# Kernel tuning notes

Measured on AMD Instinct MI355X. Metric: run time of the kernel, lower is better.

Reference implementation:

```python
import jax, jax.numpy as jnp
import numpy as np

B, S, E, H, NE, TOPK = 8, 1024, 768, 12, 8, 2
F = 4 * E
DH = E // H

def _ln(x, g, b, eps=1e-5):
    m = jnp.mean(x, axis=-1, keepdims=True)
    v = jnp.mean((x - m) ** 2, axis=-1, keepdims=True)
    return (x - m) / jnp.sqrt(v + eps) * g + b

def _expert(x, lg, lb, w1, b1, w2, b2):
    # Expert: LayerNorm -> Linear(E,4E) -> GELU(exact) -> Linear(4E,E); dropout is identity in eval
    h = _ln(x, lg, lb)
    h = jax.nn.gelu(h @ w1.T + b1, approximate=False)
    return h @ w2.T + b2

def setup_inputs():
    key = jax.random.key(0)
    ks = jax.random.split(key, 16)
    rn = lambda k, shape, s=0.02: jax.random.normal(k, shape, jnp.float32) * s
    return {
        'x': jax.random.normal(ks[0], (B, S, E), jnp.float32),
        'modality_type': jax.random.randint(ks[1], (B, S), 0, 2).astype(jnp.int32),
        'norm1_g': jnp.ones((E,), jnp.float32), 'norm1_b': jnp.zeros((E,), jnp.float32),
        'norm2_g': jnp.ones((E,), jnp.float32), 'norm2_b': jnp.zeros((E,), jnp.float32),
        'in_proj_w': rn(ks[2], (3 * E, E)), 'in_proj_b': jnp.zeros((3 * E,), jnp.float32),
        'out_proj_w': rn(ks[3], (E, E)), 'out_proj_b': jnp.zeros((E,), jnp.float32),
        'router_w': rn(ks[4], (NE, E)), 'router_b': jnp.zeros((NE,), jnp.float32),
        'spec_ln_g': jnp.ones((3, E), jnp.float32), 'spec_ln_b': jnp.zeros((3, E), jnp.float32),
        'spec_w1': rn(ks[5], (3, F, E)), 'spec_b1': jnp.zeros((3, F), jnp.float32),
        'spec_w2': rn(ks[6], (3, E, F)), 'spec_b2': jnp.zeros((3, E), jnp.float32),
        'gen_ln_g': jnp.ones((NE, E), jnp.float32), 'gen_ln_b': jnp.zeros((NE, E), jnp.float32),
        'gen_w1': rn(ks[7], (NE, F, E)), 'gen_b1': jnp.zeros((NE, F), jnp.float32),
        'gen_w2': rn(ks[8], (NE, E, F)), 'gen_b2': jnp.zeros((NE, E), jnp.float32),
    }

def _forward(x, modality_type, norm1_g, norm1_b, norm2_g, norm2_b, in_proj_w, in_proj_b,
             out_proj_w, out_proj_b, router_w, router_b,
             spec_ln_g, spec_ln_b, spec_w1, spec_b1, spec_w2, spec_b2,
             gen_ln_g, gen_ln_b, gen_w1, gen_b1, gen_w2, gen_b2):
    # --- self-attention block (pre-norm + residual), matches nn.MultiheadAttention ---
    residual = x
    xn = _ln(x, norm1_g, norm1_b)
    qkv = xn @ in_proj_w.T + in_proj_b                          # [B,S,3E]
    q, k, v = jnp.split(qkv, 3, axis=-1)
    q = q.reshape(B, S, H, DH); k = k.reshape(B, S, H, DH); v = v.reshape(B, S, H, DH)
    scores = jnp.einsum('bqhd,bkhd->bhqk', q, k) / jnp.sqrt(jnp.float32(DH))
    attn = jax.nn.softmax(scores, axis=-1)
    ctx = jnp.einsum('bhqk,bkhd->bqhd', attn, v).reshape(B, S, E)
    x = residual + (ctx @ out_proj_w.T + out_proj_b)

    # --- MoE block (pre-norm + residual) ---
    residual = x
    xn = _ln(x, norm2_g, norm2_b)
    expert_out = _expert(xn, spec_ln_g[0], spec_ln_b[0], spec_w1[0], spec_b1[0], spec_w2[0], spec_b2[0])
    # modality experts: vision on tokens with type==0, text on type==1 (not a fusion layer)
    vmask = (modality_type == 0).astype(xn.dtype)[..., None]
    tmask = (modality_type == 1).astype(xn.dtype)[..., None]
    expert_out = expert_out + vmask * _expert(xn, spec_ln_g[1], spec_ln_b[1], spec_w1[1], spec_b1[1], spec_w2[1], spec_b2[1])
    expert_out = expert_out + tmask * _expert(xn, spec_ln_g[2], spec_ln_b[2], spec_w1[2], spec_b1[2], spec_w2[2], spec_b2[2])

    # --- router: softmax -> top_k -> renormalize over top_k ---
    logits = xn @ router_w.T + router_b                         # [B,S,NE]
    probs = jax.nn.softmax(logits, axis=-1)
    topk_probs, topk_idx = jax.lax.top_k(probs, TOPK)
    topk_w = jax.nn.softmax(topk_probs, axis=-1)                # [B,S,TOPK]

    # --- dispatch/combine: per-expert combine coefficient; experts are per-token so
    # dense masked compute is mathematically identical to the torch gather/scatter loop ---
    for e in range(NE):
        coef = jnp.sum(topk_w * (topk_idx == e), axis=-1)[..., None]   # [B,S,1]
        expert_out = expert_out + coef * _expert(xn, gen_ln_g[e], gen_ln_b[e], gen_w1[e], gen_b1[e], gen_w2[e], gen_b2[e])

    return residual + expert_out

def reference(x, modality_type, norm1_g, norm1_b, norm2_g, norm2_b, in_proj_w, in_proj_b,
              out_proj_w, out_proj_b, router_w, router_b,
              spec_ln_g, spec_ln_b, spec_w1, spec_b1, spec_w2, spec_b2,
              gen_ln_g, gen_ln_b, gen_w1, gen_b1, gen_w2, gen_b2):
    return _forward(x, modality_type, norm1_g, norm1_b, norm2_g, norm2_b, in_proj_w, in_proj_b,
                    out_proj_w, out_proj_b, router_w, router_b,
                    spec_ln_g, spec_ln_b, spec_w1, spec_b1, spec_w2, spec_b2,
                    gen_ln_g, gen_ln_b, gen_w1, gen_b1, gen_w2, gen_b2)
```

## Files before the change

### kernel.cpp

```cpp
#include <hip/hip_runtime.h>
#include <cstdint>

#define NTOK 8192
#define EDIM 768
#define FDIM 3072

using bf16x8 = __attribute__((ext_vector_type(8))) __bf16;
using f32x4  = __attribute__((ext_vector_type(4))) float;

__device__ __forceinline__ float b2f(ushort u){ union{uint32_t i; float f;} v; v.i = ((uint32_t)u)<<16; return v.f; }
__device__ __forceinline__ ushort f2b(float f){ union{float f; uint32_t i;} v; v.f=f; uint32_t r = v.i + 0x7fffu + ((v.i>>16)&1u); return (ushort)(r>>16); }
__device__ __forceinline__ float gelu_f(float v){
  float c = v*(1.5957691216f + 0.0713548162726f*v*v);
  return v / (1.f + __expf(-c));
}

__global__ __launch_bounds__(256) void conv_w(const float* w0,const float* w1,const float* w2,
                                              const float* w3,const float* w4,const float* w5,
                                              const float* slg, const float* glg,
                                              ushort* pool)
{
  size_t idx4 = (size_t)blockIdx.x*256 + threadIdx.x;
  size_t e = idx4*4;
  const float* src; size_t base; int region;
  if      (e <  1769472u){src=w0;base=0;        region=0;}
  else if (e <  2359296u){src=w1;base=1769472u; region=1;}
  else if (e <  9437184u){src=w2;base=2359296u; region=2;}
  else if (e < 16515072u){src=w3;base=9437184u; region=3;}
  else if (e < 35389440u){src=w4;base=16515072u;region=4;}
  else                   {src=w5;base=35389440u;region=5;}
  size_t within = e - base;
  f32x4 f = *(const f32x4*)(src + within);
  if (region==2){
    int ex = (int)(within/2359296u); int col = (int)(within%768u);
    f32x4 g = *(const f32x4*)(slg + ex*768 + col);
    f[0]*=g[0]; f[1]*=g[1]; f[2]*=g[2]; f[3]*=g[3];
  } else if (region==4){
    int ex = (int)(within/2359296u); int col = (int)(within%768u);
    f32x4 g = *(const f32x4*)(glg + ex*768 + col);
    f[0]*=g[0]; f[1]*=g[1]; f[2]*=g[2]; f[3]*=g[3];
  }
  ushort4 u; u.x=f2b(f[0]); u.y=f2b(f[1]); u.z=f2b(f[2]); u.w=f2b(f[3]);
  *(ushort4*)(pool+e) = u;
}

__global__ __launch_bounds__(256) void b1fold_k(const float* __restrict__ sw1, const float* __restrict__ gw1,
                                                const float* __restrict__ sb1, const float* __restrict__ gb1,
                                                const float* __restrict__ slb, const float* __restrict__ glb,
                                                float* __restrict__ b1p)
{
  int j = blockIdx.x*4 + (threadIdx.x>>6);
  int lane = threadIdx.x & 63;
  int je = j / FDIM, f = j % FDIM;
  const float* wrow = (je<3) ? sw1 + ((size_t)je*FDIM + f)*EDIM : gw1 + ((size_t)(je-3)*FDIM + f)*EDIM;
  const float* lb   = (je<3) ? slb + (size_t)je*EDIM : glb + (size_t)(je-3)*EDIM;
  float s = 0.f;
  #pragma unroll
  for (int i=0;i<12;i++){ int d = lane + 64*i; s += wrow[d]*lb[d]; }
  #pragma unroll
  for (int o=32;o>0;o>>=1) s += __shfl_xor(s,o);
  if (lane==0){
    float base = (je<3) ? sb1[je*FDIM+f] : gb1[(je-3)*FDIM+f];
    b1p[j] = base + s;
  }
}

__global__ __launch_bounds__(256) void out_init(const float* __restrict__ x, const float* __restrict__ bo,
                                                float* __restrict__ out)
{
  size_t i = ((size_t)blockIdx.x*256 + threadIdx.x)*4;
  int col = (int)(i % EDIM);
  f32x4 xv = *(const f32x4*)(x+i);
  f32x4 bv = *(const f32x4*)(bo+col);
  f32x4 r = { xv[0]+bv[0], xv[1]+bv[1], xv[2]+bv[2], xv[3]+bv[3] };
  *(f32x4*)(out+i) = r;
}

__global__ __launch_bounds__(256) void ln1_k(const float* __restrict__ x, const float* __restrict__ g,
                                             const float* __restrict__ b, ushort* __restrict__ out)
{
  int w = blockIdx.x*4 + (threadIdx.x>>6);
  int lane = threadIdx.x & 63;
  const float* xr = x + (size_t)w*EDIM;
  float v[12]; float s=0.f, s2=0.f;
  #pragma unroll
  for (int i=0;i<12;i++){ v[i]=xr[lane+64*i]; s+=v[i]; s2+=v[i]*v[i]; }
  #pragma unroll
  for (int o=32;o>0;o>>=1){ s += __shfl_xor(s,o); s2 += __shfl_xor(s2,o); }
  float mu = s*(1.f/768.f);
  float rs = rsqrtf(s2*(1.f/768.f) - mu*mu + 1e-5f);
  ushort* op = out + (size_t)w*EDIM;
  #pragma unroll
  for (int i=0;i<12;i++){ int d=lane+64*i; op[d] = f2b((v[i]-mu)*rs*g[d] + b[d]); }
}

__global__ __launch_bounds__(256) void lnr_k(const float* __restrict__ x1, const float* __restrict__ g2,
                                             const float* __restrict__ b2, const float* __restrict__ rw,
                                             const float* __restrict__ rbv,
                                             ushort* __restrict__ z, float* __restrict__ coef)
{
  int w = blockIdx.x*4 + (threadIdx.x>>6);
  int lane = threadIdx.x & 63;
  const float* xr = x1 + (size_t)w*EDIM;
  float v[12]; float s=0.f, s2=0.f;
  #pragma unroll
  for (int i=0;i<12;i++){ v[i]=xr[lane+64*i]; s+=v[i]; s2+=v[i]*v[i]; }
  #pragma unroll
  for (int o=32;o>0;o>>=1){ s += __shfl_xor(s,o); s2 += __shfl_xor(s2,o); }
  float mu = s*(1.f/768.f);
  float rs = rsqrtf(s2*(1.f/768.f) - mu*mu + 1e-5f);
  float xn[12]; s=0.f; s2=0.f;
  #pragma unroll
  for (int i=0;i<12;i++){ int d=lane+64*i; xn[i]=(v[i]-mu)*rs*g2[d]+b2[d]; s+=xn[i]; s2+=xn[i]*xn[i]; }
  float pl[8] = {0.f,0.f,0.f,0.f,0.f,0.f,0.f,0.f};
  #pragma unroll
  for (int i=0;i<12;i++){
    int d=lane+64*i; float xv=xn[i];
    #pragma unroll
    for (int e=0;e<8;e++) pl[e] += xv * rw[e*EDIM + d];
  }
  #pragma unroll
  for (int o=32;o>0;o>>=1){ s += __shfl_xor(s,o); s2 += __shfl_xor(s2,o); }
  float mu2 = s*(1.f/768.f);
  float rs2 = rsqrtf(s2*(1.f/768.f) - mu2*mu2 + 1e-5f);
  ushort* op = z + (size_t)w*EDIM;
  #pragma unroll
  for (int i=0;i<12;i++){ int d=lane+64*i; op[d] = f2b((xn[i]-mu2)*rs2); }
  #pragma unroll
  for (int e=0;e<8;e++){
    #pragma unroll
    for (int o=32;o>0;o>>=1) pl[e] += __shfl_xor(pl[e], o);
  }
  float lgt[8]; float mx = -1e30f;
  #pragma unroll
  for (int e=0;e<8;e++){ lgt[e]=pl[e]+rbv[e]; mx = fmaxf(mx, lgt[e]); }
  float p[8]; float den=0.f;
  #pragma unroll
  for (int e=0;e<8;e++){ p[e]=__expf(lgt[e]-mx); den+=p[e]; }
  float inv = 1.f/den;
  #pragma unroll
  for (int e=0;e<8;e++) p[e]*=inv;
  int i1=0;
  #pragma unroll
  for (int e=1;e<8;e++) if (p[e]>p[i1]) i1=e;
  int i2=(i1==0)?1:0;
  #pragma unroll
  for (int e=0;e<8;e++){ if (e==i1) continue; if (p[e]>p[i2]) i2=e; }
  float w1 = 1.f/(1.f+__expf(p[i2]-p[i1]));
  float w2 = 1.f - w1;
  if (lane < 8){
    float c = (lane==i1)? w1 : ((lane==i2)? w2 : 0.f);
    coef[(size_t)w*8 + lane] = c;
  }
}

__global__ __launch_bounds__(256) void build_lists(const int* __restrict__ mt, const float* __restrict__ coef,
                                                   ushort* __restrict__ lists, int* __restrict__ cnt)
{
  const int job = blockIdx.x;
  ushort* list = lists + (size_t)job*NTOK;
  __shared__ int wsum[4];
  int base = 0;
  const int lane = threadIdx.x & 63, wv = threadIdx.x >> 6;
  for (int c0=0; c0<NTOK; c0+=256){
    int t = c0 + threadIdx.x;
    bool flag;
    if (job==0)      flag = (mt[t]==0);
    else if (job==1) flag = (mt[t]==1);
    else             flag = (coef[(size_t)t*8 + (job-2)] != 0.0f);
    unsigned long long bal = __ballot(flag);
    int pre = __popcll(bal & ((1ull<<lane)-1ull));
    if (lane==0) wsum[wv] = __popcll(bal);
    __syncthreads();
    int off = base + pre;
    for (int k=0;k<wv;k++) off += wsum[k];
    int tot = wsum[0]+wsum[1]+wsum[2]+wsum[3];
    if (flag) list[off] = (ushort)t;
    base += tot;
    __syncthreads();
  }
  if (threadIdx.x==0){ cnt[job+1] = base; if (job==0) cnt[0] = NTOK; }
}

struct GemmArgs {
  const ushort* A; const ushort* B;
  const float* bias;
  ushort* outBF;
  int K, ldc;
};

__global__ __launch_bounds__(256) void gemm_k(GemmArgs g)
{
  const int mb = blockIdx.x, nb = blockIdx.y;
  __shared__ __align__(16) ushort As[128*40];
  __shared__ __align__(16) ushort Bs[128*40];
  const int tid = threadIdx.x;
  const int lane = tid & 63, wave = tid >> 6;
  const int ar = tid >> 2, ac = tid & 3;
  const int row0 = mb*128 + ar, row1 = row0 + 64;
  const int KK = g.K;
  const ushort* Ap0 = g.A + (size_t)row0*KK + ac*8;
  const ushort* Ap1 = g.A + (size_t)row1*KK + ac*8;
  const ushort* Bp0 = g.B + (size_t)(nb*128+ar)*KK + ac*8;
  const ushort* Bp1 = Bp0 + (size_t)64*KK;
  const int nst = KK >> 5;
  uint4 ra0 = *(const uint4*)(Ap0);
  uint4 ra1 = *(const uint4*)(Ap1);
  uint4 rb0 = *(const uint4*)(Bp0);
  uint4 rb1 = *(const uint4*)(Bp1);
  f32x4 acc[4][4];
  #pragma unroll
  for (int m=0;m<4;m++)
    #pragma unroll
    for (int n=0;n<4;n++) acc[m][n] = (f32x4){0.f,0.f,0.f,0.f};
  const int fr = lane & 15, fq = lane >> 4;
  const int rb_ = (wave>>1)*64, cb_ = (wave&1)*64;
  for (int kt=0; kt<nst; ++kt){
    __syncthreads();
    *(uint4*)&As[ ar     *40 + ac*8] = ra0;
    *(uint4*)&As[(ar+64) *40 + ac*8] = ra1;
    *(uint4*)&Bs[ ar     *40 + ac*8] = rb0;
    *(uint4*)&Bs[(ar+64) *40 + ac*8] = rb1;
    if (kt+1 < nst){
      const int ko = (kt+1)*32;
      ra0 = *(const uint4*)(Ap0 + ko);
      ra1 = *(const uint4*)(Ap1 + ko);
      rb0 = *(const uint4*)(Bp0 + ko);
      rb1 = *(const uint4*)(Bp1 + ko);
    }
    __syncthreads();
    bf16x8 af[4], bfr[4];
    #pragma unroll
    for (int m=0;m<4;m++) af[m]  = *(const bf16x8*)&As[(rb_ + m*16 + fr)*40 + fq*8];
    #pragma unroll
    for (int n=0;n<4;n++) bfr[n] = *(const bf16x8*)&Bs[(cb_ + n*16 + fr)*40 + fq*8];
    #pragma unroll
    for (int m=0;m<4;m++)
      #pragma unroll
      for (int n=0;n<4;n++)
        acc[m][n] = __builtin_amdgcn_mfma_f32_16x16x32_bf16(af[m], bfr[n], acc[m][n], 0, 0, 0);
  }
  #pragma unroll
  for (int m=0;m<4;m++){
    #pragma unroll
    for (int j=0;j<4;j++){
      const int row = mb*128 + rb_ + m*16 + fq*4 + j;
      #pragma unroll
      for (int n=0;n<4;n++){
        const int col = nb*128 + cb_ + n*16 + fr;
        g.outBF[(size_t)row*g.ldc + col] = f2b(acc[m][n][j] + g.bias[col]);
      }
    }
  }
}

struct FArgs {
  const ushort* z; ushort* hidden; const ushort* ctx; const ushort* wo;
  float* out;
  const ushort* lists; const int* cnt; const float* coef;
  const ushort* sw1; const ushort* gw1; const ushort* sw2; const ushort* gw2;
  const float* b1p; const float* sb2; const float* gb2;
  int jobBase; int compact;
};

__device__ __forceinline__ size_t job_hoff(const FArgs& a, int job){
  size_t h = 0;
  if (a.compact){
    if (job==1) h = NTOK;
    else if (job==2) h = NTOK + (size_t)a.cnt[1];
    else if (job>=3){ for (int k=3;k<job;k++) h += (size_t)a.cnt[k]; }
  }
  return h;
}

__global__ __launch_bounds__(256) void ffn1_k(FArgs a)
{
  const int job = a.jobBase + blockIdx.z;
  const int cntj = (job==0) ? NTOK : a.cnt[job];
  const int mb = blockIdx.x, nb = blockIdx.y;
  if (mb*128 >= cntj) return;
  const ushort* list = (job==0) ? nullptr : a.lists + (size_t)(job-1)*NTOK;
  const ushort* B = (job<3) ? a.sw1+(size_t)job*FDIM*EDIM : a.gw1+(size_t)(job-3)*FDIM*EDIM;
  const float* bias = a.b1p + (size_t)job*FDIM;
  const size_t hoff = job_hoff(a, job);
  __shared__ __align__(16) ushort As[128*40];
  __shared__ __align__(16) ushort Bs[128*40];
  const int tid = threadIdx.x;
  const int lane = tid & 63, wave = tid >> 6;
  const int ar = tid >> 2, ac = tid & 3;
  const int row0 = mb*128 + ar, row1 = row0 + 64;
  const int t0 = list ? (int)list[min(row0,cntj-1)] : min(row0,cntj-1);
  const int t1 = list ? (int)list[min(row1,cntj-1)] : min(row1,cntj-1);
  const ushort* Ap0 = a.z + (size_t)t0*EDIM + ac*8;
  const ushort* Ap1 = a.z + (size_t)t1*EDIM + ac*8;
  const ushort* Bp0 = B + (size_t)(nb*128+ar)*EDIM + ac*8;
  const ushort* Bp1 = Bp0 + (size_t)64*EDIM;
  uint4 ra0 = *(const uint4*)(Ap0);
  uint4 ra1 = *(const uint4*)(Ap1);
  uint4 rb0 = *(const uint4*)(Bp0);
  uint4 rb1 = *(const uint4*)(Bp1);
  f32x4 acc[4][4];
  #pragma unroll
  for (int m=0;m<4;m++)
    #pragma unroll
    for (int n=0;n<4;n++) acc[m][n] = (f32x4){0.f,0.f,0.f,0.f};
  const int fr = lane & 15, fq = lane >> 4;
  const int rb_ = (wave>>1)*64, cb_ = (wave&1)*64;
  for (int kt=0; kt<24; ++kt){
    __syncthreads();
    *(uint4*)&As[ ar     *40 + ac*8] = ra0;
    *(uint4*)&As[(ar+64) *40 + ac*8] = ra1;
    *(uint4*)&Bs[ ar     *40 + ac*8] = rb0;
    *(uint4*)&Bs[(ar+64) *40 + ac*8] = rb1;
    if (kt+1 < 24){
      const int ko = (kt+1)*32;
      ra0 = *(const uint4*)(Ap0 + ko);
      ra1 = *(const uint4*)(Ap1 + ko);
      rb0 = *(const uint4*)(Bp0 + ko);
      rb1 = *(const uint4*)(Bp1 + ko);
    }
    __syncthreads();
    bf16x8 af[4], bfr[4];
    #pragma unroll
    for (int m=0;m<4;m++) af[m]  = *(const bf16x8*)&As[(rb_ + m*16 + fr)*40 + fq*8];
    #pragma unroll
    for (int n=0;n<4;n++) bfr[n] = *(const bf16x8*)&Bs[(cb_ + n*16 + fr)*40 + fq*8];
    #pragma unroll
    for (int m=0;m<4;m++)
      #pragma unroll
      for (int n=0;n<4;n++)
        acc[m][n] = __builtin_amdgcn_mfma_f32_16x16x32_bf16(af[m], bfr[n], acc[m][n], 0, 0, 0);
  }
  #pragma unroll
  for (int m=0;m<4;m++){
    #pragma unroll
    for (int j=0;j<4;j++){
      const int row = mb*128 + rb_ + m*16 + fq*4 + j;
      if (row < cntj){
        #pragma unroll
        for (int n=0;n<4;n++){
          const int col = nb*128 + cb_ + n*16 + fr;
          a.hidden[(hoff+row)*FDIM + col] = f2b(gelu_f(acc[m][n][j] + bias[col]));
        }
      }
    }
  }
}

__global__ __launch_bounds__(256) void ffn2_k(FArgs a)
{
  const int zb = blockIdx.z;
  const bool op = (a.jobBase < 0);
  const int job = op ? -1 : a.jobBase + (zb>>1);
  const int ks = zb & 1;
  const int cntj = op ? NTOK : ((job==0) ? NTOK : a.cnt[job]);
  const int mb = blockIdx.x, nb = blockIdx.y;
  if (mb*128 >= cntj) return;
  const ushort* list = (op || job==0) ? nullptr : a.lists + (size_t)(job-1)*NTOK;
  const ushort* Abase; int lda; const ushort* B; const float* bias = nullptr;
  const float* coefp = nullptr; int eidx = 0; int kLen;
  if (op){ Abase = a.ctx; lda = EDIM; B = a.wo; kLen = EDIM/2; }
  else {
    lda = FDIM; kLen = FDIM/2;
    Abase = a.hidden + job_hoff(a, job)*FDIM;
    if (job<3){ B=a.sw2+(size_t)job*(size_t)EDIM*FDIM; bias=a.sb2+(size_t)job*EDIM; }
    else { eidx=job-3; B=a.gw2+(size_t)eidx*(size_t)EDIM*FDIM; bias=a.gb2+(size_t)eidx*EDIM; coefp=a.coef; }
  }
  const int kOff = ks*kLen;
  const int nst = kLen >> 5;
  __shared__ __align__(16) ushort As[128*40];
  __shared__ __align__(16) ushort Bs[128*40];
  const int tid = threadIdx.x;
  const int lane = tid & 63, wave = tid >> 6;
  const int ar = tid >> 2, ac = tid & 3;
  const int row0 = mb*128 + ar, row1 = row0 + 64;
  const ushort* Ap0 = Abase + (size_t)min(row0,cntj-1)*lda + kOff + ac*8;
  const ushort* Ap1 = Abase + (size_t)min(row1,cntj-1)*lda + kOff + ac*8;
  const ushort* Bp0 = B + (size_t)(nb*128+ar)*lda + kOff + ac*8;
  const ushort* Bp1 = Bp0 + (size_t)64*lda;
  uint4 ra0 = *(const uint4*)(Ap0);
  uint4 ra1 = *(const uint4*)(Ap1);
  uint4 rb0 = *(const uint4*)(Bp0);
  uint4 rb1 = *(const uint4*)(Bp1);
  f32x4 acc[4][4];
  #pragma unroll
  for (int m=0;m<4;m++)
    #pragma unroll
    for (int n=0;n<4;n++) acc[m][n] = (f32x4){0.f,0.f,0.f,0.f};
  const int fr = lane & 15, fq = lane >> 4;
  const int rb_ = (wave>>1)*64, cb_ = (wave&1)*64;
  for (int kt=0; kt<nst; ++kt){
    __syncthreads();
    *(uint4*)&As[ ar     *40 + ac*8] = ra0;
    *(uint4*)&As[(ar+64) *40 + ac*8] = ra1;
    *(uint4*)&Bs[ ar     *40 + ac*8] = rb0;
    *(uint4*)&Bs[(ar+64) *40 + ac*8] = rb1;
    if (kt+1 < nst){
      const int ko = (kt+1)*32;
      ra0 = *(const uint4*)(Ap0 + ko);
      ra1 = *(const uint4*)(Ap1 + ko);
      rb0 = *(const uint4*)(Bp0 + ko);
      rb1 = *(const uint4*)(Bp1 + ko);
    }
    __syncthreads();
    bf16x8 af[4], bfr[4];
    #pragma unroll
    for (int m=0;m<4;m++) af[m]  = *(const bf16x8*)&As[(rb_ + m*16 + fr)*40 + fq*8];
    #pragma unroll
    for (int n=0;n<4;n++) bfr[n] = *(const bf16x8*)&Bs[(cb_ + n*16 + fr)*40 + fq*8];
    #pragma unroll
    for (int m=0;m<4;m++)
      #pragma unroll
      for (int n=0;n<4;n++)
        acc[m][n] = __builtin_amdgcn_mfma_f32_16x16x32_bf16(af[m], bfr[n], acc[m][n], 0, 0, 0);
  }
  #pragma unroll
  for (int m=0;m<4;m++){
    #pragma unroll
    for (int j=0;j<4;j++){
      const int row = mb*128 + rb_ + m*16 + fq*4 + j;
      if (row < cntj){
        const int tok = list ? (int)list[row] : row;
        const float c = coefp ? coefp[(size_t)tok*8 + eidx] : 1.0f;
        #pragma unroll
        for (int n=0;n<4;n++){
          const int col = nb*128 + cb_ + n*16 + fr;
          float v = acc[m][n][j];
          if (bias && ks==0) v += bias[col];
          atomicAdd(&a.out[(size_t)tok*EDIM + col], c*v);
        }
      }
    }
  }
}

__global__ __launch_bounds__(256) void attn_k(const ushort* __restrict__ qkv, ushort* __restrict__ ctx)
{
  const int qb = blockIdx.x, bh = blockIdx.y;
  const int b = bh/12, h = bh%12;
  const int tid = threadIdx.x;
  const int lane = tid & 63, w = tid >> 6;
  const int fr = lane & 15, fq = lane >> 4;
  __shared__ __align__(16) ushort Ks[4096];
  __shared__ __align__(16) ushort Vts[4096];
  __shared__ __align__(16) ushort Ps[4096];
  const size_t tokq = (size_t)b*1024 + (size_t)qb*64;

  bf16x8 qf[2];
  {
    const ushort* qp = qkv + (tokq + w*16 + fr)*2304 + h*64 + fq*8;
    qf[0] = *(const bf16x8*)(qp);
    qf[1] = *(const bf16x8*)(qp + 32);
  }
  f32x4 o[4];
  #pragma unroll
  for (int nt=0;nt<4;nt++) o[nt] = (f32x4){0.f,0.f,0.f,0.f};
  float m[4] = {-1e30f,-1e30f,-1e30f,-1e30f};
  float l[4] = {0.f,0.f,0.f,0.f};

  const int skr = tid>>3, skc = (tid&7)*8;
  const int svd = (tid&15)*4, svk = (tid>>4)*4;

  for (int kt=0; kt<16; ++kt){
    __syncthreads();
    const size_t tokk = (size_t)b*1024 + (size_t)kt*64;
    #pragma unroll
    for (int p=0;p<2;p++){
      int row = skr + p*32;
      uint4 kq = *(const uint4*)(qkv + (tokk+row)*2304 + 768 + h*64 + skc);
      *(uint4*)&Ks[row*64 + (skc ^ ((row&7)<<3))] = kq;
    }
    {
      union { ushort4 v4[4]; ushort s[16]; } tv;
      #pragma unroll
      for (int i=0;i<4;i++)
        tv.v4[i] = *(const ushort4*)(qkv + (tokk+svk+i)*2304 + 1536 + h*64 + svd);
      #pragma unroll
      for (int j=0;j<4;j++){
        ushort4 tj; tj.x=tv.s[j]; tj.y=tv.s[4+j]; tj.z=tv.s[8+j]; tj.w=tv.s[12+j];
        int dr = svd + j;
        *(ushort4*)&Vts[dr*64 + (svk ^ ((dr&7)<<3))] = tj;
      }
    }
    __syncthreads();
    f32x4 s[4];
    #pragma unroll
    for (int nt=0;nt<4;nt++){
      s[nt] = (f32x4){0.f,0.f,0.f,0.f};
      int kr = nt*16 + fr;
      const ushort* kb = &Ks[kr*64];
      int sw = (kr&7)<<3;
      bf16x8 k0 = *(const bf16x8*)&kb[(fq*8) ^ sw];
      bf16x8 k1 = *(const bf16x8*)&kb[(fq*8+32) ^ sw];
      s[nt] = __builtin_amdgcn_mfma_f32_16x16x32_bf16(qf[0], k0, s[nt], 0,0,0);
      s[nt] = __builtin_amdgcn_mfma_f32_16x16x32_bf16(qf[1], k1, s[nt], 0,0,0);
    }
    float a_[4], pr[4][4];
    #pragma unroll
    for (int j=0;j<4;j++){
      float mx = fmaxf(fmaxf(s[0][j],s[1][j]), fmaxf(s[2][j],s[3][j])) * 0.125f;
      mx = fmaxf(mx, __shfl_xor(mx,1));
      mx = fmaxf(mx, __shfl_xor(mx,2));
      mx = fmaxf(mx, __shfl_xor(mx,4));
      mx = fmaxf(mx, __shfl_xor(mx,8));
      float mn = fmaxf(m[j], mx);
      float a = __expf(m[j] - mn);
      m[j] = mn; a_[j] = a;
      float ss = 0.f;
      #pragma unroll
      for (int nt=0;nt<4;nt++){
        float p = __expf(s[nt][j]*0.125f - mn);
        pr[nt][j] = p; ss += p;
      }
      ss += __shfl_xor(ss,1);
      ss += __shfl_xor(ss,2);
      ss += __shfl_xor(ss,4);
      ss += __shfl_xor(ss,8);
      l[j] = l[j]*a + ss;
    }
    #pragma unroll
    for (int nt=0;nt<4;nt++){
      #pragma unroll
      for (int j=0;j<4;j++){
        int row = fq*4 + j;
        Ps[w*1024 + row*64 + ((nt*16+fr) ^ ((row&7)<<3))] = f2b(pr[nt][j]);
        o[nt][j] *= a_[j];
      }
    }
    #pragma unroll
    for (int ks=0; ks<2; ++ks){
      int kvo = ks*32 + fq*8;
      bf16x8 pf = *(const bf16x8*)&Ps[w*1024 + fr*64 + (kvo ^ ((fr&7)<<3))];
      #pragma unroll
      for (int nt=0;nt<4;nt++){
        int dr = nt*16 + fr;
        bf16x8 vf = *(const bf16x8*)&Vts[dr*64 + (kvo ^ ((dr&7)<<3))];
        o[nt] = __builtin_amdgcn_mfma_f32_16x16x32_bf16(pf, vf, o[nt], 0,0,0);
      }
    }
  }
  float inv[4];
  #pragma unroll
  for (int j=0;j<4;j++) inv[j] = 1.f/l[j];
  ushort* cp = ctx + (tokq + w*16)*768 + h*64;
  #pragma unroll
  for (int nt=0;nt<4;nt++){
    #pragma unroll
    for (int j=0;j<4;j++){
      cp[(size_t)(fq*4+j)*768 + nt*16 + fr] = f2b(o[nt][j]*inv[j]);
    }
  }
}

#define OFF_POOL   0u
#define OFF_Z      108527616u
#define OFF_COEF   121110528u
#define OFF_LISTS  121372672u
#define OFF_CNT    121536512u
#define OFF_B1P    121536768u
#define OFF_QKV    121700608u
#define OFF_CTX    159449344u
#define OFF_XN1    172032256u
#define WS_GROUPED  222363904u

extern "C" void kernel_launch(void* const* d_in, const int* in_sizes, int n_in,
                              void* d_out, int out_size, void* d_ws, size_t ws_size,
                              hipStream_t stream)
{
  const float* x    = (const float*)d_in[0];
  const int*   mt   = (const int*)d_in[1];
  const float* n1g  = (const float*)d_in[2];
  const float* n1b  = (const float*)d_in[3];
  const float* n2g  = (const float*)d_in[4];
  const float* n2b  = (const float*)d_in[5];
  const float* wqkv = (const float*)d_in[6];
  const float* bqkv = (const float*)d_in[7];
  const float* wo   = (const float*)d_in[8];
  const float* bo   = (const float*)d_in[9];
  const float* rw   = (const float*)d_in[10];
  const float* rb   = (const float*)d_in[11];
  const float* slg  = (const float*)d_in[12];
  const float* slb  = (const float*)d_in[13];
  const float* sw1  = (const float*)d_in[14];
  const float* sb1  = (const float*)d_in[15];
  const float* sw2  = (const float*)d_in[16];
  const float* sb2  = (const float*)d_in[17];
  const float* glg  = (const float*)d_in[18];
  const float* glb  = (const float*)d_in[19];
  const float* gw1  = (const float*)d_in[20];
  const float* gb1  = (const float*)d_in[21];
  const float* gw2  = (const float*)d_in[22];
  const float* gb2  = (const float*)d_in[23];
  float* out = (float*)d_out;
  char* ws = (char*)d_ws;

  ushort* pool  = (ushort*)(ws + OFF_POOL);
  ushort* z     = (ushort*)(ws + OFF_Z);
  float*  coef  = (float*) (ws + OFF_COEF);
  ushort* lists = (ushort*)(ws + OFF_LISTS);
  int*    cnt   = (int*)   (ws + OFF_CNT);
  float*  b1p   = (float*) (ws + OFF_B1P);
  ushort* qkv   = (ushort*)(ws + OFF_QKV);
  ushort* ctx   = (ushort*)(ws + OFF_CTX);
  ushort* xn1   = (ushort*)(ws + OFF_XN1);
  ushort* hidden= (ushort*)(ws + OFF_QKV);

  ushort* pWqkv = pool + 0;
  ushort* pWo   = pool + 1769472;
  ushort* pSw1  = pool + 2359296;
  ushort* pSw2  = pool + 9437184;
  ushort* pGw1  = pool + 16515072;
  ushort* pGw2  = pool + 35389440;

  const bool grouped = (ws_size >= (size_t)WS_GROUPED);

  conv_w<<<52992, 256, 0, stream>>>(wqkv, wo, sw1, sw2, gw1, gw2, slg, glg, pool);
  b1fold_k<<<8448, 256, 0, stream>>>(sw1, gw1, sb1, gb1, slb, glb, b1p);
  ln1_k<<<2048, 256, 0, stream>>>(x, n1g, n1b, xn1);
  { GemmArgs a{}; a.A=xn1; a.B=pWqkv; a.bias=bqkv; a.outBF=qkv; a.K=768; a.ldc=2304;
    gemm_k<<<dim3(64,18),256,0,stream>>>(a); }
  attn_k<<<dim3(16,96),256,0,stream>>>(qkv, ctx);
  out_init<<<6144,256,0,stream>>>(x, bo, out);

  FArgs fa{};
  fa.z=z; fa.hidden=hidden; fa.ctx=ctx; fa.wo=pWo; fa.out=out;
  fa.lists=lists; fa.cnt=cnt; fa.coef=coef;
  fa.sw1=pSw1; fa.gw1=pGw1; fa.sw2=pSw2; fa.gw2=pGw2;
  fa.b1p=b1p; fa.sb2=sb2; fa.gb2=gb2;

  { FArgs a = fa; a.jobBase = -1; a.compact = 0;
    ffn2_k<<<dim3(64,6,2),256,0,stream>>>(a); }

  lnr_k<<<2048,256,0,stream>>>(out, n2g, n2b, rw, rb, z, coef);
  build_lists<<<10,256,0,stream>>>(mt, coef, lists, cnt);

  if (grouped){
    { FArgs a = fa; a.jobBase = 0; a.compact = 1;
      ffn1_k<<<dim3(64,24,3),256,0,stream>>>(a);
      ffn2_k<<<dim3(64,6,6),256,0,stream>>>(a); }
    { FArgs a = fa; a.jobBase = 3; a.compact = 1;
      ffn1_k<<<dim3(64,24,8),256,0,stream>>>(a);
      ffn2_k<<<dim3(64,6,16),256,0,stream>>>(a); }
  } else {
    for (int j=0;j<11;j++){
      FArgs a = fa; a.jobBase = j; a.compact = 0;
      ffn1_k<<<dim3(64,24,1),256,0,stream>>>(a);
      ffn2_k<<<dim3(64,6,2),256,0,stream>>>(a);
    }
  }
}
```

Baseline: 1.155 ms.

## Use direct global-to-LDS loads with XOR swizzle and drop split-K in FFN2

Replaces the register-staged global→LDS copy in all three GEMM kernels with global_load_lds 16-byte direct loads into an unpadded, XOR-swizzled LDS tile, which removes VGPR staging and LDS write instructions. FFN2 no longer splits K across two blocks, so each output tile is reduced in a single pass. The output projection now uses a plain read-modify-write in place of atomics. In exchange, the explicit register prefetch of the next tile is gone, so global load latency is exposed inside each iteration between the two barriers. Removing split-K also halves the FFN2 grid, reducing parallelism.

```diff
diff --git a/kernel.cpp b/kernel.cpp
--- a/kernel.cpp
+++ b/kernel.cpp
@@ -13,6 +13,11 @@
 __device__ __forceinline__ float gelu_f(float v){
   float c = v*(1.5957691216f + 0.0713548162726f*v*v);
   return v / (1.f + __expf(-c));
+}
+
+__device__ __forceinline__ void gload16(const ushort* g, ushort* l){
+  __builtin_amdgcn_global_load_lds((const __attribute__((address_space(1))) void*)g,
+                                   (__attribute__((address_space(3))) void*)l, 16, 0, 0);
 }
 
 __global__ __launch_bounds__(256) void conv_w(const float* w0,const float* w1,const float* w2,
@@ -192,48 +197,43 @@
 __global__ __launch_bounds__(256) void gemm_k(GemmArgs g)
 {
   const int mb = blockIdx.x, nb = blockIdx.y;
-  __shared__ __align__(16) ushort As[128*40];
-  __shared__ __align__(16) ushort Bs[128*40];
+  __shared__ __align__(1024) ushort As[128*32];
+  __shared__ __align__(1024) ushort Bs[128*32];
   const int tid = threadIdx.x;
-  const int lane = tid & 63, wave = tid >> 6;
-  const int ar = tid >> 2, ac = tid & 3;
-  const int row0 = mb*128 + ar, row1 = row0 + 64;
+  const int lane = tid & 63, w = tid >> 6;
+  const int seg = lane & 3;
+  const int lrow = w*16 + (lane>>2);
+  const int p = (lane>>3)&3;
+  ushort* ldsA0 = As + (size_t)w*512;
+  ushort* ldsA1 = As + (size_t)(w+4)*512;
+  ushort* ldsB0 = Bs + (size_t)w*512;
+  ushort* ldsB1 = Bs + (size_t)(w+4)*512;
   const int KK = g.K;
-  const ushort* Ap0 = g.A + (size_t)row0*KK + ac*8;
-  const ushort* Ap1 = g.A + (size_t)row1*KK + ac*8;
-  const ushort* Bp0 = g.B + (size_t)(nb*128+ar)*KK + ac*8;
-  const ushort* Bp1 = Bp0 + (size_t)64*KK;
+  const ushort* pA0 = g.A + (size_t)(mb*128 + lrow)*KK + (seg^p)*8;
+  const ushort* pA1 = pA0 + (size_t)64*KK;
+  const ushort* pB0 = g.B + (size_t)(nb*128 + lrow)*KK + (seg^p)*8;
+  const ushort* pB1 = pB0 + (size_t)64*KK;
   const int nst = KK >> 5;
-  uint4 ra0 = *(const uint4*)(Ap0);
-  uint4 ra1 = *(const uint4*)(Ap1);
-  uint4 rb0 = *(const uint4*)(Bp0);
-  uint4 rb1 = *(const uint4*)(Bp1);
   f32x4 acc[4][4];
   #pragma unroll
   for (int m=0;m<4;m++)
     #pragma unroll
     for (int n=0;n<4;n++) acc[m][n] = (f32x4){0.f,0.f,0.f,0.f};
   const int fr = lane & 15, fq = lane >> 4;
-  const int rb_ = (wave>>1)*64, cb_ = (wave&1)*64;
+  const int pr = (fr>>1)&3;
+  const int so = (fq^pr)*8;
+  const int rb_ = (w>>1)*64, cb_ = (w&1)*64;
   for (int kt=0; kt<nst; ++kt){
     __syncthreads();
-    *(uint4*)&As[ ar     *40 + ac*8] = ra0;
-    *(uint4*)&As[(ar+64) *40 + ac*8] = ra1;
-    *(uint4*)&Bs[ ar     *40 + ac*8] = rb0;
-    *(uint4*)&Bs[(ar+64) *40 + ac*8] = rb1;
-    if (kt+1 < nst){
-      const int ko = (kt+1)*32;
-      ra0 = *(const uint4*)(Ap0 + ko);
-      ra1 = *(const uint4*)(Ap1 + ko);
-      rb0 = *(const uint4*)(Bp0 + ko);
-      rb1 = *(const uint4*)(Bp1 + ko);
-    }
+    gload16(pA0, ldsA0); gload16(pA1, ldsA1);
+    gload16(pB0, ldsB0); gload16(pB1, ldsB1);
+    pA0 += 32; pA1 += 32; pB0 += 32; pB1 += 32;
     __syncthreads();
     bf16x8 af[4], bfr[4];
     #pragma unroll
-    for (int m=0;m<4;m++) af[m]  = *(const bf16x8*)&As[(rb_ + m*16 + fr)*40 + fq*8];
-    #pragma unroll
-    for (int n=0;n<4;n++) bfr[n] = *(const bf16x8*)&Bs[(cb_ + n*16 + fr)*40 + fq*8];
+    for (int m=0;m<4;m++) af[m]  = *(const bf16x8*)&As[(rb_ + m*16 + fr)*32 + so];
+    #pragma unroll
+    for (int n=0;n<4;n++) bfr[n] = *(const bf16x8*)&Bs[(cb_ + n*16 + fr)*32 + so];
     #pragma unroll
     for (int m=0;m<4;m++)
       #pragma unroll
@@ -283,48 +283,44 @@
   const ushort* B = (job<3) ? a.sw1+(size_t)job*FDIM*EDIM : a.gw1+(size_t)(job-3)*FDIM*EDIM;
   const float* bias = a.b1p + (size_t)job*FDIM;
   const size_t hoff = job_hoff(a, job);
-  __shared__ __align__(16) ushort As[128*40];
-  __shared__ __align__(16) ushort Bs[128*40];
+  __shared__ __align__(1024) ushort As[128*32];
+  __shared__ __align__(1024) ushort Bs[128*32];
   const int tid = threadIdx.x;
-  const int lane = tid & 63, wave = tid >> 6;
-  const int ar = tid >> 2, ac = tid & 3;
-  const int row0 = mb*128 + ar, row1 = row0 + 64;
-  const int t0 = list ? (int)list[min(row0,cntj-1)] : min(row0,cntj-1);
-  const int t1 = list ? (int)list[min(row1,cntj-1)] : min(row1,cntj-1);
-  const ushort* Ap0 = a.z + (size_t)t0*EDIM + ac*8;
-  const ushort* Ap1 = a.z + (size_t)t1*EDIM + ac*8;
-  const ushort* Bp0 = B + (size_t)(nb*128+ar)*EDIM + ac*8;
-  const ushort* Bp1 = Bp0 + (size_t)64*EDIM;
-  uint4 ra0 = *(const uint4*)(Ap0);
-  uint4 ra1 = *(const uint4*)(Ap1);
-  uint4 rb0 = *(const uint4*)(Bp0);
-  uint4 rb1 = *(const uint4*)(Bp1);
+  const int lane = tid & 63, w = tid >> 6;
+  const int seg = lane & 3;
+  const int lrow = w*16 + (lane>>2);
+  const int p = (lane>>3)&3;
+  ushort* ldsA0 = As + (size_t)w*512;
+  ushort* ldsA1 = As + (size_t)(w+4)*512;
+  ushort* ldsB0 = Bs + (size_t)w*512;
+  ushort* ldsB1 = Bs + (size_t)(w+4)*512;
+  const int r0 = mb*128 + lrow, r1 = r0 + 64;
+  const int tA0 = list ? (int)list[min(r0,cntj-1)] : min(r0,cntj-1);
+  const int tA1 = list ? (int)list[min(r1,cntj-1)] : min(r1,cntj-1);
+  const ushort* pA0 = a.z + (size_t)tA0*EDIM + (seg^p)*8;
+  const ushort* pA1 = a.z + (size_t)tA1*EDIM + (seg^p)*8;
+  const ushort* pB0 = B + (size_t)(nb*128 + lrow)*EDIM + (seg^p)*8;
+  const ushort* pB1 = pB0 + (size_t)64*EDIM;
   f32x4 acc[4][4];
   #pragma unroll
   for (int m=0;m<4;m++)
     #pragma unroll
     for (int n=0;n<4;n++) acc[m][n] = (f32x4){0.f,0.f,0.f,0.f};
   const int fr = lane & 15, fq = lane >> 4;
-  const int rb_ = (wave>>1)*64, cb_ = (wave&1)*64;
+  const int pr = (fr>>1)&3;
+  const int so = (fq^pr)*8;
+  const int rb_ = (w>>1)*64, cb_ = (w&1)*64;
   for (int kt=0; kt<24; ++kt){
     __syncthreads();
-    *(uint4*)&As[ ar     *40 + ac*8] = ra0;
-    *(uint4*)&As[(ar+64) *40 + ac*8] = ra1;
-    *(uint4*)&Bs[ ar     *40 + ac*8] = rb0;
-    *(uint4*)&Bs[(ar+64) *40 + ac*8] = rb1;
-    if (kt+1 < 24){
-      const int ko = (kt+1)*32;
-      ra0 = *(const uint4*)(Ap0 + ko);
-      ra1 = *(const uint4*)(Ap1 + ko);
-      rb0 = *(const uint4*)(Bp0 + ko);
-      rb1 = *(const uint4*)(Bp1 + ko);
-    }
+    gload16(pA0, ldsA0); gload16(pA1, ldsA1);
+    gload16(pB0, ldsB0); gload16(pB1, ldsB1);
+    pA0 += 32; pA1 += 32; pB0 += 32; pB1 += 32;
     __syncthreads();
     bf16x8 af[4], bfr[4];
     #pragma unroll
-    for (int m=0;m<4;m++) af[m]  = *(const bf16x8*)&As[(rb_ + m*16 + fr)*40 + fq*8];
-    #pragma unroll
-    for (int n=0;n<4;n++) bfr[n] = *(const bf16x8*)&Bs[(cb_ + n*16 + fr)*40 + fq*8];
+    for (int m=0;m<4;m++) af[m]  = *(const bf16x8*)&As[(rb_ + m*16 + fr)*32 + so];
+    #pragma unroll
+    for (int n=0;n<4;n++) bfr[n] = *(const bf16x8*)&Bs[(cb_ + n*16 + fr)*32 + so];
     #pragma unroll
     for (int m=0;m<4;m++)
       #pragma unroll
@@ -349,65 +345,58 @@
 
 __global__ __launch_bounds__(256) void ffn2_k(FArgs a)
 {
-  const int zb = blockIdx.z;
   const bool op = (a.jobBase < 0);
-  const int job = op ? -1 : a.jobBase + (zb>>1);
-  const int ks = zb & 1;
+  const int job = op ? -1 : a.jobBase + blockIdx.z;
   const int cntj = op ? NTOK : ((job==0) ? NTOK : a.cnt[job]);
   const int mb = blockIdx.x, nb = blockIdx.y;
   if (mb*128 >= cntj) return;
   const ushort* list = (op || job==0) ? nullptr : a.lists + (size_t)(job-1)*NTOK;
   const ushort* Abase; int lda; const ushort* B; const float* bias = nullptr;
-  const float* coefp = nullptr; int eidx = 0; int kLen;
-  if (op){ Abase = a.ctx; lda = EDIM; B = a.wo; kLen = EDIM/2; }
+  const float* coefp = nullptr; int eidx = 0;
+  if (op){ Abase = a.ctx; lda = EDIM; B = a.wo; }
   else {
-    lda = FDIM; kLen = FDIM/2;
+    lda = FDIM;
     Abase = a.hidden + job_hoff(a, job)*FDIM;
     if (job<3){ B=a.sw2+(size_t)job*(size_t)EDIM*FDIM; bias=a.sb2+(size_t)job*EDIM; }
     else { eidx=job-3; B=a.gw2+(size_t)eidx*(size_t)EDIM*FDIM; bias=a.gb2+(size_t)eidx*EDIM; coefp=a.coef; }
   }
-  const int kOff = ks*kLen;
-  const int nst = kLen >> 5;
-  __shared__ __align__(16) ushort As[128*40];
-  __shared__ __align__(16) ushort Bs[128*40];
+  const int nst = lda >> 5;
+  __shared__ __align__(1024) ushort As[128*32];
+  __shared__ __align__(1024) ushort Bs[128*32];
   const int tid = threadIdx.x;
-  const int lane = tid & 63, wave = tid >> 6;
-  const int ar = tid >> 2, ac = tid & 3;
-  const int row0 = mb*128 + ar, row1 = row0 + 64;
-  const ushort* Ap0 = Abase + (size_t)min(row0,cntj-1)*lda + kOff + ac*8;
-  const ushort* Ap1 = Abase + (size_t)min(row1,cntj-1)*lda + kOff + ac*8;
-  const ushort* Bp0 = B + (size_t)(nb*128+ar)*lda + kOff + ac*8;
-  const ushort* Bp1 = Bp0 + (size_t)64*lda;
-  uint4 ra0 = *(const uint4*)(Ap0);
-  uint4 ra1 = *(const uint4*)(Ap1);
-  uint4 rb0 = *(const uint4*)(Bp0);
-  uint4 rb1 = *(const uint4*)(Bp1);
+  const int lane = tid & 63, w = tid >> 6;
+  const int seg = lane & 3;
+  const int lrow = w*16 + (lane>>2);
+  const int p = (lane>>3)&3;
+  ushort* ldsA0 = As + (size_t)w*512;
+  ushort* ldsA1 = As + (size_t)(w+4)*512;
+  ushort* ldsB0 = Bs + (size_t)w*512;
+  ushort* ldsB1 = Bs + (size_t)(w+4)*512;
+  const int r0 = mb*128 + lrow, r1 = r0 + 64;
+  const ushort* pA0 = Abase + (size_t)min(r0,cntj-1)*lda + (seg^p)*8;
+  const ushort* pA1 = Abase + (size_t)min(r1,cntj-1)*lda + (seg^p)*8;
+  const ushort* pB0 = B + (size_t)(nb*128 + lrow)*lda + (seg^p)*8;
+  const ushort* pB1 = pB0 + (size_t)64*lda;
   f32x4 acc[4][4];
   #pragma unroll
   for (int m=0;m<4;m++)
     #pragma unroll
     for (int n=0;n<4;n++) acc[m][n] = (f32x4){0.f,0.f,0.f,0.f};
   const int fr = lane & 15, fq = lane >> 4;
-  const int rb_ = (wave>>1)*64, cb_ = (wave&1)*64;
+  const int pr = (fr>>1)&3;
+  const int so = (fq^pr)*8;
+  const int rb_ = (w>>1)*64, cb_ = (w&1)*64;
   for (int kt=0; kt<nst; ++kt){
     __syncthreads();
-    *(uint4*)&As[ ar     *40 + ac*8] = ra0;
-    *(uint4*)&As[(ar+64) *40 + ac*8] = ra1;
-    *(uint4*)&Bs[ ar     *40 + ac*8] = rb0;
-    *(uint4*)&Bs[(ar+64) *40 + ac*8] = rb1;
-    if (kt+1 < nst){
-      const int ko = (kt+1)*32;
-      ra0 = *(const uint4*)(Ap0 + ko);
-      ra1 = *(const uint4*)(Ap1 + ko);
-      rb0 = *(const uint4*)(Bp0 + ko);
-      rb1 = *(const uint4*)(Bp1 + ko);
-    }
+    gload16(pA0, ldsA0); gload16(pA1, ldsA1);
+    gload16(pB0, ldsB0); gload16(pB1, ldsB1);
+    pA0 += 32; pA1 += 32; pB0 += 32; pB1 += 32;
     __syncthreads();
     bf16x8 af[4], bfr[4];
     #pragma unroll
-    for (int m=0;m<4;m++) af[m]  = *(const bf16x8*)&As[(rb_ + m*16 + fr)*40 + fq*8];
-    #pragma unroll
-    for (int n=0;n<4;n++) bfr[n] = *(const bf16x8*)&Bs[(cb_ + n*16 + fr)*40 + fq*8];
+    for (int m=0;m<4;m++) af[m]  = *(const bf16x8*)&As[(rb_ + m*16 + fr)*32 + so];
+    #pragma unroll
+    for (int n=0;n<4;n++) bfr[n] = *(const bf16x8*)&Bs[(cb_ + n*16 + fr)*32 + so];
     #pragma unroll
     for (int m=0;m<4;m++)
       #pragma unroll
@@ -426,8 +415,10 @@
         for (int n=0;n<4;n++){
           const int col = nb*128 + cb_ + n*16 + fr;
           float v = acc[m][n][j];
-          if (bias && ks==0) v += bias[col];
-          atomicAdd(&a.out[(size_t)tok*EDIM + col], c*v);
+          if (bias) v += bias[col];
+          float* dst = &a.out[(size_t)tok*EDIM + col];
+          if (op) *dst += v;
+          else atomicAdd(dst, c*v);
         }
       }
     }
@@ -465,8 +456,8 @@
     __syncthreads();
     const size_t tokk = (size_t)b*1024 + (size_t)kt*64;
     #pragma unroll
-    for (int p=0;p<2;p++){
-      int row = skr + p*32;
+    for (int pp=0;pp<2;pp++){
+      int row = skr + pp*32;
       uint4 kq = *(const uint4*)(qkv + (tokk+row)*2304 + 768 + h*64 + skc);
       *(uint4*)&Ks[row*64 + (skc ^ ((row&7)<<3))] = kq;
     }
@@ -504,19 +495,19 @@
       mx = fmaxf(mx, __shfl_xor(mx,4));
       mx = fmaxf(mx, __shfl_xor(mx,8));
       float mn = fmaxf(m[j], mx);
-      float a = __expf(m[j] - mn);
-      m[j] = mn; a_[j] = a;
+      float aa = __expf(m[j] - mn);
+      m[j] = mn; a_[j] = aa;
       float ss = 0.f;
       #pragma unroll
       for (int nt=0;nt<4;nt++){
-        float p = __expf(s[nt][j]*0.125f - mn);
-        pr[nt][j] = p; ss += p;
+        float pv = __expf(s[nt][j]*0.125f - mn);
+        pr[nt][j] = pv; ss += pv;
       }
       ss += __shfl_xor(ss,1);
       ss += __shfl_xor(ss,2);
       ss += __shfl_xor(ss,4);
       ss += __shfl_xor(ss,8);
-      l[j] = l[j]*a + ss;
+      l[j] = l[j]*aa + ss;
     }
     #pragma unroll
     for (int nt=0;nt<4;nt++){
@@ -629,7 +620,7 @@
   fa.b1p=b1p; fa.sb2=sb2; fa.gb2=gb2;
 
   { FArgs a = fa; a.jobBase = -1; a.compact = 0;
-    ffn2_k<<<dim3(64,6,2),256,0,stream>>>(a); }
+    ffn2_k<<<dim3(64,6,1),256,0,stream>>>(a); }
 
   lnr_k<<<2048,256,0,stream>>>(out, n2g, n2b, rw, rb, z, coef);
   build_lists<<<10,256,0,stream>>>(mt, coef, lists, cnt);
@@ -637,15 +628,15 @@
   if (grouped){
     { FArgs a = fa; a.jobBase = 0; a.compact = 1;
       ffn1_k<<<dim3(64,24,3),256,0,stream>>>(a);
-      ffn2_k<<<dim3(64,6,6),256,0,stream>>>(a); }
+      ffn2_k<<<dim3(64,6,3),256,0,stream>>>(a); }
     { FArgs a = fa; a.jobBase = 3; a.compact = 1;
       ffn1_k<<<dim3(64,24,8),256,0,stream>>>(a);
-      ffn2_k<<<dim3(64,6,16),256,0,stream>>>(a); }
+      ffn2_k<<<dim3(64,6,8),256,0,stream>>>(a); }
   } else {
     for (int j=0;j<11;j++){
       FArgs a = fa; a.jobBase = j; a.compact = 0;
       ffn1_k<<<dim3(64,24,1),256,0,stream>>>(a);
-      ffn2_k<<<dim3(64,6,2),256,0,stream>>>(a);
-    }
-  }
-}
+      ffn2_k<<<dim3(64,6,1),256,0,stream>>>(a);
+    }
+  }
+}
```

Result: slower. 1.201 ms (+3.9%).
